# Optimization experiments

Measured on AMD Instinct MI355X. Metric: run time of the kernel, lower is better.

Reference implementation:

```python
import jax, jax.numpy as jnp
import numpy as np

D_IN = 1024
D_OUT = 1024
NUM_HEADS = 16
HEAD_DIM = D_OUT // NUM_HEADS


def setup_inputs() -> dict:
    key = jax.random.key(0)
    k_x, k_q, k_k, k_v, k_o, k_ob = jax.random.split(key, 6)
    s_in = 1.0 / np.sqrt(D_IN)
    s_out = 1.0 / np.sqrt(D_OUT)
    return {
        "x": jax.random.normal(k_x, (2, 2048, D_IN), dtype=jnp.float32),
        "W_q": jax.random.uniform(k_q, (D_IN, D_OUT), minval=-s_in, maxval=s_in, dtype=jnp.float32),
        "W_k": jax.random.uniform(k_k, (D_IN, D_OUT), minval=-s_in, maxval=s_in, dtype=jnp.float32),
        "W_v": jax.random.uniform(k_v, (D_IN, D_OUT), minval=-s_in, maxval=s_in, dtype=jnp.float32),
        "W_out": jax.random.uniform(k_o, (D_OUT, D_OUT), minval=-s_out, maxval=s_out, dtype=jnp.float32),
        "b_out": jax.random.uniform(k_ob, (D_OUT,), minval=-s_out, maxval=s_out, dtype=jnp.float32),
    }


def reference(x, W_q, W_k, W_v, W_out, b_out):
    b, t, _ = x.shape
    # projections (qkv_bias=False)
    q = (x @ W_q).reshape(b, t, NUM_HEADS, HEAD_DIM).transpose(0, 2, 1, 3)  # [b,h,t,d]
    k = (x @ W_k).reshape(b, t, NUM_HEADS, HEAD_DIM).transpose(0, 2, 1, 3)
    v = (x @ W_v).reshape(b, t, NUM_HEADS, HEAD_DIM).transpose(0, 2, 1, 3)
    scale = 1.0 / np.sqrt(HEAD_DIM).astype(np.float32)
    scores = jnp.einsum("bhqd,bhkd->bhqk", q, k) * scale  # [b,h,t,t]
    causal = jnp.triu(jnp.ones((t, t), dtype=bool), k=1)
    scores = jnp.where(causal, -jnp.inf, scores)
    weights = jax.nn.softmax(scores, axis=-1)
    # dropout p=0.0 -> identity
    context = jnp.einsum("bhqk,bhkd->bhqd", weights, v)
    context = context.transpose(0, 2, 1, 3).reshape(b, t, D_OUT)
    return context @ W_out + b_out
```

## Files before the change

### kernel.cpp

```cpp
#include <hip/hip_runtime.h>
#include <hip/hip_bf16.h>

#define B_  2
#define T_  2048
#define D_  1024
#define H_  16
#define DH_ 64
#define M_  (B_*T_)

typedef _Float16 f16;
typedef __attribute__((ext_vector_type(4))) _Float16 f16x4;
typedef __attribute__((ext_vector_type(8))) _Float16 f16x8;
typedef __attribute__((ext_vector_type(4))) float f32x4;

#define GLOAD_LDS(gp, lp) __builtin_amdgcn_global_load_lds( \
    (const __attribute__((address_space(1))) void*)(gp),    \
    (__attribute__((address_space(3))) void*)(lp), 16, 0, 0)

__global__ void cvt_x(const float* __restrict__ x, f16* __restrict__ xb) {
  size_t i = ((size_t)blockIdx.x * blockDim.x + threadIdx.x) * 8;
  float4 a = *(const float4*)(x + i);
  float4 b = *(const float4*)(x + i + 4);
  f16x8 o;
  o[0]=(f16)a.x; o[1]=(f16)a.y; o[2]=(f16)a.z; o[3]=(f16)a.w;
  o[4]=(f16)b.x; o[5]=(f16)b.y; o[6]=(f16)b.z; o[7]=(f16)b.w;
  *(f16x8*)(xb + i) = o;
}

__global__ void twt(const float* __restrict__ wq, const float* __restrict__ wk,
                    const float* __restrict__ wv, const float* __restrict__ wo,
                    f16* __restrict__ wqkvT, f16* __restrict__ woutT) {
  int j = blockIdx.z;
  const float* src = (j==0)?wq:(j==1)?wk:(j==2)?wv:wo;
  f16* dst = (j<3) ? (wqkvT + (size_t)j*D_*D_) : woutT;
  __shared__ float tile[32][33];
  int n0 = blockIdx.x*32, k0 = blockIdx.y*32;
  int tx = threadIdx.x, ty = threadIdx.y;
  #pragma unroll
  for (int i=0;i<32;i+=8)
    tile[ty+i][tx] = src[(size_t)(k0+ty+i)*D_ + n0+tx];
  __syncthreads();
  #pragma unroll
  for (int i=0;i<32;i+=8)
    dst[(size_t)(n0+ty+i)*D_ + k0+tx] = (f16)tile[tx][ty+i];
}

__launch_bounds__(256, 2)
__global__ void qkv_gemm(const f16* __restrict__ xb, const f16* __restrict__ wT,
                         f16* __restrict__ Qp, f16* __restrict__ Kp, f16* __restrict__ Vtp) {
  const int j  = blockIdx.z;
  const f16* B0 = wT + (size_t)j * D_ * D_;
  const int m0 = blockIdx.y * 128;
  const int n0 = blockIdx.x * 128;
  __shared__ alignas(16) char smem[128*136*2];
  f16* AsF = (f16*)smem;
  f16* BsF = AsF + 128*64;
  const int tid = threadIdx.x;
  const int lane = tid & 63, wave = tid >> 6;
  const int ln = lane & 15, quad = lane >> 4;
  const int wm = wave >> 1, wn = wave & 1;

  f32x4 acc[4][4];
  #pragma unroll
  for (int a=0;a<4;++a)
    #pragma unroll
    for (int b=0;b<4;++b) acc[a][b] = f32x4{0.f,0.f,0.f,0.f};

  const bool swapped = (j < 2);
  for (int k0 = 0; k0 < D_; k0 += 64) {
    #pragma unroll
    for (int p = 0; p < 4; ++p) {
      int slot = p*256 + tid;
      int row  = slot >> 3;
      int c    = (slot & 7) ^ (row & 7);
      GLOAD_LDS(xb + (size_t)(m0+row)*D_ + k0 + c*8, AsF + (size_t)slot*8);
      GLOAD_LDS(B0 + (size_t)(n0+row)*D_ + k0 + c*8, BsF + (size_t)slot*8);
    }
    __syncthreads();
    #pragma unroll
    for (int ks = 0; ks < 2; ++ks) {
      const int cb = ((ks*4 + quad) ^ (ln & 7)) * 8;
      f16x8 af[4], bf[4];
      #pragma unroll
      for (int mt = 0; mt < 4; ++mt)
        af[mt] = *(const f16x8*)(AsF + (size_t)(wm*64 + mt*16 + ln)*64 + cb);
      #pragma unroll
      for (int nt = 0; nt < 4; ++nt)
        bf[nt] = *(const f16x8*)(BsF + (size_t)(wn*64 + nt*16 + ln)*64 + cb);
      if (swapped) {
        #pragma unroll
        for (int nt = 0; nt < 4; ++nt)
          #pragma unroll
          for (int mt = 0; mt < 4; ++mt)
            acc[nt][mt] = __builtin_amdgcn_mfma_f32_16x16x32_f16(bf[nt], af[mt], acc[nt][mt], 0, 0, 0);
      } else {
        #pragma unroll
        for (int mt = 0; mt < 4; ++mt)
          #pragma unroll
          for (int nt = 0; nt < 4; ++nt)
            acc[mt][nt] = __builtin_amdgcn_mfma_f32_16x16x32_f16(af[mt], bf[nt], acc[mt][nt], 0, 0, 0);
      }
    }
    __syncthreads();
  }

  if (swapped) {
    const float scale = (j == 0) ? 0.125f : 1.0f;
    f16* dstB = (j == 0) ? Qp : Kp;
    #pragma unroll
    for (int nt = 0; nt < 4; ++nt)
      #pragma unroll
      for (int mt = 0; mt < 4; ++mt) {
        int gm = m0 + wm*64 + mt*16 + ln;
        int gn = n0 + wn*64 + nt*16 + quad*4;
        int bb = gm >> 11, t = gm & (T_-1);
        int h  = gn >> 6,  dd = gn & (DH_-1);
        f16x4 v;
        #pragma unroll
        for (int r = 0; r < 4; ++r) v[r] = (f16)(acc[nt][mt][r] * scale);
        *(f16x4*)&dstB[((((size_t)bb*H_ + h)*T_ + t)*DH_) + dd] = v;
      }
  } else {
    __syncthreads();
    f16* VtS = (f16*)smem;
    #pragma unroll
    for (int mt = 0; mt < 4; ++mt)
      #pragma unroll
      for (int nt = 0; nt < 4; ++nt) {
        f16x4 v;
        v[0]=(f16)acc[mt][nt][0]; v[1]=(f16)acc[mt][nt][1];
        v[2]=(f16)acc[mt][nt][2]; v[3]=(f16)acc[mt][nt][3];
        *(f16x4*)&VtS[(size_t)(wn*64 + nt*16 + ln)*136 + wm*64 + mt*16 + quad*4] = v;
      }
    __syncthreads();
    int dd_loc = tid >> 1, half = tid & 1;
    int gn = n0 + dd_loc, h = gn >> 6, dd = gn & (DH_-1);
    int bb = m0 >> 11, tb = (m0 & (T_-1)) + half*64;
    f16* dst = Vtp + ((size_t)(bb*H_ + h)*DH_ + dd)*T_ + tb;
    const f16* src = VtS + (size_t)dd_loc*136 + half*64;
    #pragma unroll
    for (int u = 0; u < 8; ++u)
      *(uint4*)(dst + u*8) = *(const uint4*)(src + u*8);
  }
}

__launch_bounds__(256, 3)
__global__ void flash(const f16* __restrict__ Qp, const f16* __restrict__ Kp,
                      const f16* __restrict__ Vtp, f16* __restrict__ ctx) {
  const int p  = blockIdx.x;
  const int bh = blockIdx.y;
  const int b = bh >> 4, h = bh & (H_-1);
  const f16* Kh = Kp  + (size_t)bh * T_ * DH_;
  const f16* Vh = Vtp + (size_t)bh * DH_ * T_;
  const f16* Qh = Qp  + (size_t)bh * T_ * DH_;
  const int tid = threadIdx.x, lane = tid & 63, w = tid >> 6;
  const int ln = lane & 15, quad = lane >> 4;
  __shared__ alignas(16) f16 Ks[2*64*64];
  __shared__ alignas(16) f16 Vs[2*64*64];
  __shared__ alignas(16) f16 Ps[64][72];

  #pragma unroll 1
  for (int phase = 0; phase < 2; ++phase) {
    const int qt = phase ? (31 - p) : p;
    const int qw = qt*64 + w*16;

    f16x8 qf[2];
    #pragma unroll
    for (int ks = 0; ks < 2; ++ks)
      qf[ks] = *(const f16x8*)&Qh[(size_t)(qw + ln)*DH_ + ks*32 + quad*8];

    f32x4 o[4];
    #pragma unroll
    for (int dt = 0; dt < 4; ++dt) o[dt] = f32x4{0.f,0.f,0.f,0.f};
    float l_part = 0.f;

    {
      #pragma unroll
      for (int i = 0; i < 2; ++i) {
        int row = w*16 + i*8 + (lane >> 3);
        int c   = (lane & 7) ^ (row & 7);
        GLOAD_LDS(Kh + (size_t)row*DH_ + c*8, Ks + (w*128 + i*64 + lane)*8);
        GLOAD_LDS(Vh + (size_t)row*T_  + c*8, Vs + (w*128 + i*64 + lane)*8);
      }
    }
    __syncthreads();

    for (int it = 0; it <= qt; ++it) {
      const f16* Kc = Ks + (it & 1)*4096;
      const f16* Vc = Vs + (it & 1)*4096;
      if (it < qt) {
        const int kv1 = (it + 1)*64;
        f16* Kn = Ks + ((it + 1) & 1)*4096;
        f16* Vn = Vs + ((it + 1) & 1)*4096;
        #pragma unroll
        for (int i = 0; i < 2; ++i) {
          int row = w*16 + i*8 + (lane >> 3);
          int c   = (lane & 7) ^ (row & 7);
          GLOAD_LDS(Kh + (size_t)(kv1 + row)*DH_ + c*8, Kn + (w*128 + i*64 + lane)*8);
          GLOAD_LDS(Vh + (size_t)row*T_ + kv1 + c*8,    Vn + (w*128 + i*64 + lane)*8);
        }
      }

      f32x4 s[4];
      #pragma unroll
      for (int kt = 0; kt < 4; ++kt) s[kt] = f32x4{0.f,0.f,0.f,0.f};
      #pragma unroll
      for (int ks = 0; ks < 2; ++ks) {
        f16x8 kx[4];
        #pragma unroll
        for (int kt = 0; kt < 4; ++kt)
          kx[kt] = *(const f16x8*)(Kc + (size_t)(kt*16 + ln)*64 + (((ks*4 + quad) ^ (ln & 7))*8));
        #pragma unroll
        for (int kt = 0; kt < 4; ++kt)
          s[kt] = __builtin_amdgcn_mfma_f32_16x16x32_f16(kx[kt], qf[ks], s[kt], 0, 0, 0);
      }
      if (it == qt) {
        const int kv0 = it*64;
        #pragma unroll
        for (int kt = 0; kt < 4; ++kt)
          #pragma unroll
          for (int r = 0; r < 4; ++r)
            if (kv0 + kt*16 + quad*4 + r > qw + ln) s[kt][r] = -INFINITY;
      }
      #pragma unroll
      for (int kt = 0; kt < 4; ++kt) {
        f16x4 pk;
        #pragma unroll
        for (int r = 0; r < 4; ++r) {
          float pe = __expf(s[kt][r]);
          l_part += pe;
          pk[r] = (f16)pe;
        }
        *(f16x4*)&Ps[w*16 + ln][kt*16 + quad*4] = pk;
      }
      asm volatile("" ::: "memory");

      #pragma unroll
      for (int ks = 0; ks < 2; ++ks) {
        f16x8 px = *(const f16x8*)&Ps[w*16 + ln][ks*32 + quad*8];
        #pragma unroll
        for (int dt = 0; dt < 4; ++dt) {
          f16x8 vy = *(const f16x8*)(Vc + (size_t)(dt*16 + ln)*64 + (((ks*4 + quad) ^ (ln & 7))*8));
          o[dt] = __builtin_amdgcn_mfma_f32_16x16x32_f16(px, vy, o[dt], 0, 0, 0);
        }
      }
      __syncthreads();
    }

    float l = l_part;
    l += __shfl_xor(l, 16, 64);
    l += __shfl_xor(l, 32, 64);
    float inv = 1.0f / l;
    #pragma unroll
    for (int r = 0; r < 4; ++r) {
      float linv = __shfl(inv, quad*4 + r, 64);
      int t = qt*64 + w*16 + quad*4 + r;
      #pragma unroll
      for (int dt = 0; dt < 4; ++dt)
        ctx[(size_t)(b*T_ + t)*D_ + h*DH_ + dt*16 + ln] = (f16)(o[dt][r] * linv);
    }
  }
}

__launch_bounds__(256, 2)
__global__ void out_gemm(const f16* __restrict__ ctx, const f16* __restrict__ woT,
                         const float* __restrict__ bo, float* __restrict__ out) {
  const int m0 = blockIdx.y * 128;
  const int n0 = blockIdx.x * 128;
  __shared__ alignas(16) f16 smem[2*128*64];
  f16* AsF = smem;
  f16* BsF = AsF + 128*64;
  const int tid = threadIdx.x;
  const int lane = tid & 63, wave = tid >> 6;
  const int ln = lane & 15, quad = lane >> 4;
  const int wm = wave >> 1, wn = wave & 1;

  f32x4 acc[4][4];
  #pragma unroll
  for (int a=0;a<4;++a)
    #pragma unroll
    for (int b=0;b<4;++b) acc[a][b] = f32x4{0.f,0.f,0.f,0.f};

  for (int k0 = 0; k0 < D_; k0 += 64) {
    #pragma unroll
    for (int p = 0; p < 4; ++p) {
      int slot = p*256 + tid;
      int row  = slot >> 3;
      int c    = (slot & 7) ^ (row & 7);
      GLOAD_LDS(ctx + (size_t)(m0+row)*D_ + k0 + c*8, AsF + (size_t)slot*8);
      GLOAD_LDS(woT + (size_t)(n0+row)*D_ + k0 + c*8, BsF + (size_t)slot*8);
    }
    __syncthreads();
    #pragma unroll
    for (int ks = 0; ks < 2; ++ks) {
      const int cb = ((ks*4 + quad) ^ (ln & 7)) * 8;
      f16x8 af[4], bf[4];
      #pragma unroll
      for (int mt = 0; mt < 4; ++mt)
        af[mt] = *(const f16x8*)(AsF + (size_t)(wm*64 + mt*16 + ln)*64 + cb);
      #pragma unroll
      for (int nt = 0; nt < 4; ++nt)
        bf[nt] = *(const f16x8*)(BsF + (size_t)(wn*64 + nt*16 + ln)*64 + cb);
      #pragma unroll
      for (int nt = 0; nt < 4; ++nt)
        #pragma unroll
        for (int mt = 0; mt < 4; ++mt)
          acc[nt][mt] = __builtin_amdgcn_mfma_f32_16x16x32_f16(bf[nt], af[mt], acc[nt][mt], 0, 0, 0);
    }
    __syncthreads();
  }

  #pragma unroll
  for (int nt = 0; nt < 4; ++nt) {
    int gn = n0 + wn*64 + nt*16 + quad*4;
    float4 bv = *(const float4*)&bo[gn];
    #pragma unroll
    for (int mt = 0; mt < 4; ++mt) {
      int gm = m0 + wm*64 + mt*16 + ln;
      float4 v;
      v.x = acc[nt][mt][0] + bv.x;
      v.y = acc[nt][mt][1] + bv.y;
      v.z = acc[nt][mt][2] + bv.z;
      v.w = acc[nt][mt][3] + bv.w;
      *(float4*)&out[(size_t)gm*D_ + gn] = v;
    }
  }
}

extern "C" void kernel_launch(void* const* d_in, const int* in_sizes, int n_in,
                              void* d_out, int out_size, void* d_ws, size_t ws_size,
                              hipStream_t stream) {
  const float* x  = (const float*)d_in[0];
  const float* wq = (const float*)d_in[1];
  const float* wk = (const float*)d_in[2];
  const float* wv = (const float*)d_in[3];
  const float* wo = (const float*)d_in[4];
  const float* bo = (const float*)d_in[5];
  float* out = (float*)d_out;

  f16* ws    = (f16*)d_ws;
  f16* xb    = ws;
  f16* wqkvT = xb    + (size_t)M_*D_;
  f16* woutT = wqkvT + (size_t)3*D_*D_;
  f16* Qb    = woutT + (size_t)D_*D_;
  f16* Kb    = Qb    + (size_t)M_*D_;
  f16* Vb    = Kb    + (size_t)M_*D_;
  f16* ctx   = Vb    + (size_t)M_*D_;

  cvt_x<<<(M_*D_)/(256*8), 256, 0, stream>>>(x, xb);
  twt<<<dim3(D_/32, D_/32, 4), dim3(32, 8), 0, stream>>>(wq, wk, wv, wo, wqkvT, woutT);
  qkv_gemm<<<dim3(D_/128, M_/128, 3), 256, 0, stream>>>(xb, wqkvT, Qb, Kb, Vb);
  flash<<<dim3(16, 32), 256, 0, stream>>>(Qb, Kb, Vb, ctx);
  out_gemm<<<dim3(D_/128, M_/128), 256, 0, stream>>>(ctx, woutT, bo, out);
}
```

Baseline: 190.8 us.

## Double-buffer LDS tiles in GEMMs and remap block indices for cache locality

Both projection GEMMs now double-buffer their A/B tiles in shared memory, prefetching the next K slice with global_load_lds while MFMAs run on the current one. This removes one barrier per K step and hides load latency, at the cost of doubling LDS to 64KB per block, which may limit occupancy. Launches move to flat 1D grids with a swizzled mapping that groups blocks sharing the same weight or head panel, aiming for better L2 reuse. The flash grid is reordered so consecutive blocks cover different heads.

```diff
diff --git a/kernel.cpp b/kernel.cpp
--- a/kernel.cpp
+++ b/kernel.cpp
@@ -48,13 +48,15 @@
 __launch_bounds__(256, 2)
 __global__ void qkv_gemm(const f16* __restrict__ xb, const f16* __restrict__ wT,
                          f16* __restrict__ Qp, f16* __restrict__ Kp, f16* __restrict__ Vtp) {
-  const int j  = blockIdx.z;
+  const int fid = blockIdx.x;
+  const int g = fid & 7, r = fid >> 3;
+  const int m0 = ((((r & 3) << 3) | g)) * 128;
+  const int n0 = ((r >> 2) & 7) * 128;
+  const int j  = r >> 5;
   const f16* B0 = wT + (size_t)j * D_ * D_;
-  const int m0 = blockIdx.y * 128;
-  const int n0 = blockIdx.x * 128;
-  __shared__ alignas(16) char smem[128*136*2];
+  __shared__ alignas(16) char smem[65536];
   f16* AsF = (f16*)smem;
-  f16* BsF = AsF + 128*64;
+  f16* BsF = AsF + 2*128*64;
   const int tid = threadIdx.x;
   const int lane = tid & 63, wave = tid >> 6;
   const int ln = lane & 15, quad = lane >> 4;
@@ -67,26 +69,45 @@
     for (int b=0;b<4;++b) acc[a][b] = f32x4{0.f,0.f,0.f,0.f};
 
   const bool swapped = (j < 2);
-  for (int k0 = 0; k0 < D_; k0 += 64) {
-    #pragma unroll
-    for (int p = 0; p < 4; ++p) {
-      int slot = p*256 + tid;
-      int row  = slot >> 3;
-      int c    = (slot & 7) ^ (row & 7);
-      GLOAD_LDS(xb + (size_t)(m0+row)*D_ + k0 + c*8, AsF + (size_t)slot*8);
-      GLOAD_LDS(B0 + (size_t)(n0+row)*D_ + k0 + c*8, BsF + (size_t)slot*8);
-    }
-    __syncthreads();
+
+  const int slot_row[4] = { (0*256+tid)>>3, (1*256+tid)>>3, (2*256+tid)>>3, (3*256+tid)>>3 };
+
+  #pragma unroll
+  for (int p = 0; p < 4; ++p) {
+    int slot = p*256 + tid;
+    int row  = slot_row[p];
+    int c    = (slot & 7) ^ (row & 7);
+    GLOAD_LDS(xb + (size_t)(m0+row)*D_ + c*8, AsF + (size_t)slot*8);
+    GLOAD_LDS(B0 + (size_t)(n0+row)*D_ + c*8, BsF + (size_t)slot*8);
+  }
+  __syncthreads();
+
+  for (int it = 0; it < 16; ++it) {
+    const f16* Ac = AsF + (it & 1)*8192;
+    const f16* Bc = BsF + (it & 1)*8192;
+    if (it < 15) {
+      const int k1 = (it + 1) * 64;
+      f16* An = AsF + ((it + 1) & 1)*8192;
+      f16* Bn = BsF + ((it + 1) & 1)*8192;
+      #pragma unroll
+      for (int p = 0; p < 4; ++p) {
+        int slot = p*256 + tid;
+        int row  = slot_row[p];
+        int c    = (slot & 7) ^ (row & 7);
+        GLOAD_LDS(xb + (size_t)(m0+row)*D_ + k1 + c*8, An + (size_t)slot*8);
+        GLOAD_LDS(B0 + (size_t)(n0+row)*D_ + k1 + c*8, Bn + (size_t)slot*8);
+      }
+    }
     #pragma unroll
     for (int ks = 0; ks < 2; ++ks) {
       const int cb = ((ks*4 + quad) ^ (ln & 7)) * 8;
       f16x8 af[4], bf[4];
       #pragma unroll
       for (int mt = 0; mt < 4; ++mt)
-        af[mt] = *(const f16x8*)(AsF + (size_t)(wm*64 + mt*16 + ln)*64 + cb);
+        af[mt] = *(const f16x8*)(Ac + (size_t)(wm*64 + mt*16 + ln)*64 + cb);
       #pragma unroll
       for (int nt = 0; nt < 4; ++nt)
-        bf[nt] = *(const f16x8*)(BsF + (size_t)(wn*64 + nt*16 + ln)*64 + cb);
+        bf[nt] = *(const f16x8*)(Bc + (size_t)(wn*64 + nt*16 + ln)*64 + cb);
       if (swapped) {
         #pragma unroll
         for (int nt = 0; nt < 4; ++nt)
@@ -117,11 +138,10 @@
         int h  = gn >> 6,  dd = gn & (DH_-1);
         f16x4 v;
         #pragma unroll
-        for (int r = 0; r < 4; ++r) v[r] = (f16)(acc[nt][mt][r] * scale);
+        for (int rr = 0; rr < 4; ++rr) v[rr] = (f16)(acc[nt][mt][rr] * scale);
         *(f16x4*)&dstB[((((size_t)bb*H_ + h)*T_ + t)*DH_) + dd] = v;
       }
   } else {
-    __syncthreads();
     f16* VtS = (f16*)smem;
     #pragma unroll
     for (int mt = 0; mt < 4; ++mt)
@@ -147,8 +167,9 @@
 __launch_bounds__(256, 3)
 __global__ void flash(const f16* __restrict__ Qp, const f16* __restrict__ Kp,
                       const f16* __restrict__ Vtp, f16* __restrict__ ctx) {
-  const int p  = blockIdx.x;
-  const int bh = blockIdx.y;
+  const int fid = blockIdx.x;
+  const int bh = fid & 31;
+  const int p  = fid >> 5;
   const int b = bh >> 4, h = bh & (H_-1);
   const f16* Kh = Kp  + (size_t)bh * T_ * DH_;
   const f16* Vh = Vtp + (size_t)bh * DH_ * T_;
@@ -174,14 +195,12 @@
     for (int dt = 0; dt < 4; ++dt) o[dt] = f32x4{0.f,0.f,0.f,0.f};
     float l_part = 0.f;
 
-    {
-      #pragma unroll
-      for (int i = 0; i < 2; ++i) {
-        int row = w*16 + i*8 + (lane >> 3);
-        int c   = (lane & 7) ^ (row & 7);
-        GLOAD_LDS(Kh + (size_t)row*DH_ + c*8, Ks + (w*128 + i*64 + lane)*8);
-        GLOAD_LDS(Vh + (size_t)row*T_  + c*8, Vs + (w*128 + i*64 + lane)*8);
-      }
+    #pragma unroll
+    for (int i = 0; i < 2; ++i) {
+      int row = w*16 + i*8 + (lane >> 3);
+      int c   = (lane & 7) ^ (row & 7);
+      GLOAD_LDS(Kh + (size_t)row*DH_ + c*8, Ks + (w*128 + i*64 + lane)*8);
+      GLOAD_LDS(Vh + (size_t)row*T_  + c*8, Vs + (w*128 + i*64 + lane)*8);
     }
     __syncthreads();
 
@@ -219,17 +238,17 @@
         #pragma unroll
         for (int kt = 0; kt < 4; ++kt)
           #pragma unroll
-          for (int r = 0; r < 4; ++r)
-            if (kv0 + kt*16 + quad*4 + r > qw + ln) s[kt][r] = -INFINITY;
+          for (int rr = 0; rr < 4; ++rr)
+            if (kv0 + kt*16 + quad*4 + rr > qw + ln) s[kt][rr] = -INFINITY;
       }
       #pragma unroll
       for (int kt = 0; kt < 4; ++kt) {
         f16x4 pk;
         #pragma unroll
-        for (int r = 0; r < 4; ++r) {
-          float pe = __expf(s[kt][r]);
+        for (int rr = 0; rr < 4; ++rr) {
+          float pe = __expf(s[kt][rr]);
           l_part += pe;
-          pk[r] = (f16)pe;
+          pk[rr] = (f16)pe;
         }
         *(f16x4*)&Ps[w*16 + ln][kt*16 + quad*4] = pk;
       }
@@ -252,12 +271,12 @@
     l += __shfl_xor(l, 32, 64);
     float inv = 1.0f / l;
     #pragma unroll
-    for (int r = 0; r < 4; ++r) {
-      float linv = __shfl(inv, quad*4 + r, 64);
-      int t = qt*64 + w*16 + quad*4 + r;
+    for (int rr = 0; rr < 4; ++rr) {
+      float linv = __shfl(inv, quad*4 + rr, 64);
+      int t = qt*64 + w*16 + quad*4 + rr;
       #pragma unroll
       for (int dt = 0; dt < 4; ++dt)
-        ctx[(size_t)(b*T_ + t)*D_ + h*DH_ + dt*16 + ln] = (f16)(o[dt][r] * linv);
+        ctx[(size_t)(b*T_ + t)*D_ + h*DH_ + dt*16 + ln] = (f16)(o[dt][rr] * linv);
     }
   }
 }
@@ -265,11 +284,13 @@
 __launch_bounds__(256, 2)
 __global__ void out_gemm(const f16* __restrict__ ctx, const f16* __restrict__ woT,
                          const float* __restrict__ bo, float* __restrict__ out) {
-  const int m0 = blockIdx.y * 128;
-  const int n0 = blockIdx.x * 128;
-  __shared__ alignas(16) f16 smem[2*128*64];
+  const int fid = blockIdx.x;
+  const int g = fid & 7, r = fid >> 3;
+  const int m0 = ((((r & 3) << 3) | g)) * 128;
+  const int n0 = (r >> 2) * 128;
+  __shared__ alignas(16) f16 smem[4*128*64];
   f16* AsF = smem;
-  f16* BsF = AsF + 128*64;
+  f16* BsF = AsF + 2*128*64;
   const int tid = threadIdx.x;
   const int lane = tid & 63, wave = tid >> 6;
   const int ln = lane & 15, quad = lane >> 4;
@@ -281,26 +302,42 @@
     #pragma unroll
     for (int b=0;b<4;++b) acc[a][b] = f32x4{0.f,0.f,0.f,0.f};
 
-  for (int k0 = 0; k0 < D_; k0 += 64) {
-    #pragma unroll
-    for (int p = 0; p < 4; ++p) {
-      int slot = p*256 + tid;
-      int row  = slot >> 3;
-      int c    = (slot & 7) ^ (row & 7);
-      GLOAD_LDS(ctx + (size_t)(m0+row)*D_ + k0 + c*8, AsF + (size_t)slot*8);
-      GLOAD_LDS(woT + (size_t)(n0+row)*D_ + k0 + c*8, BsF + (size_t)slot*8);
-    }
-    __syncthreads();
+  #pragma unroll
+  for (int p = 0; p < 4; ++p) {
+    int slot = p*256 + tid;
+    int row  = slot >> 3;
+    int c    = (slot & 7) ^ (row & 7);
+    GLOAD_LDS(ctx + (size_t)(m0+row)*D_ + c*8, AsF + (size_t)slot*8);
+    GLOAD_LDS(woT + (size_t)(n0+row)*D_ + c*8, BsF + (size_t)slot*8);
+  }
+  __syncthreads();
+
+  for (int it = 0; it < 16; ++it) {
+    const f16* Ac = AsF + (it & 1)*8192;
+    const f16* Bc = BsF + (it & 1)*8192;
+    if (it < 15) {
+      const int k1 = (it + 1) * 64;
+      f16* An = AsF + ((it + 1) & 1)*8192;
+      f16* Bn = BsF + ((it + 1) & 1)*8192;
+      #pragma unroll
+      for (int p = 0; p < 4; ++p) {
+        int slot = p*256 + tid;
+        int row  = slot >> 3;
+        int c    = (slot & 7) ^ (row & 7);
+        GLOAD_LDS(ctx + (size_t)(m0+row)*D_ + k1 + c*8, An + (size_t)slot*8);
+        GLOAD_LDS(woT + (size_t)(n0+row)*D_ + k1 + c*8, Bn + (size_t)slot*8);
+      }
+    }
     #pragma unroll
     for (int ks = 0; ks < 2; ++ks) {
       const int cb = ((ks*4 + quad) ^ (ln & 7)) * 8;
       f16x8 af[4], bf[4];
       #pragma unroll
       for (int mt = 0; mt < 4; ++mt)
-        af[mt] = *(const f16x8*)(AsF + (size_t)(wm*64 + mt*16 + ln)*64 + cb);
+        af[mt] = *(const f16x8*)(Ac + (size_t)(wm*64 + mt*16 + ln)*64 + cb);
       #pragma unroll
       for (int nt = 0; nt < 4; ++nt)
-        bf[nt] = *(const f16x8*)(BsF + (size_t)(wn*64 + nt*16 + ln)*64 + cb);
+        bf[nt] = *(const f16x8*)(Bc + (size_t)(wn*64 + nt*16 + ln)*64 + cb);
       #pragma unroll
       for (int nt = 0; nt < 4; ++nt)
         #pragma unroll
@@ -349,7 +386,7 @@
 
   cvt_x<<<(M_*D_)/(256*8), 256, 0, stream>>>(x, xb);
   twt<<<dim3(D_/32, D_/32, 4), dim3(32, 8), 0, stream>>>(wq, wk, wv, wo, wqkvT, woutT);
-  qkv_gemm<<<dim3(D_/128, M_/128, 3), 256, 0, stream>>>(xb, wqkvT, Qb, Kb, Vb);
-  flash<<<dim3(16, 32), 256, 0, stream>>>(Qb, Kb, Vb, ctx);
-  out_gemm<<<dim3(D_/128, M_/128), 256, 0, stream>>>(ctx, woutT, bo, out);
-}
+  qkv_gemm<<<768, 256, 0, stream>>>(xb, wqkvT, Qb, Kb, Vb);
+  flash<<<512, 256, 0, stream>>>(Qb, Kb, Vb, ctx);
+  out_gemm<<<256, 256, 0, stream>>>(ctx, woutT, bo, out);
+}
```

After: 172.3 us. 9.7% less time.
